# Performance work log

Measured on AMD Instinct MI355X. Metric: run time of the kernel, lower is better.

The kernel has to match this reference:

```python
import jax, jax.numpy as jnp
import numpy as np

N, T, H, W, C = 8, 128, 32, 32, 3
HID = 128
CONV_F = 32
FLAT = H * W * CONV_F  # 32768


def setup_inputs() -> dict:
    key = jax.random.key(0)
    ks = jax.random.split(key, 8)
    def w(k, shape, fan_in):
        return jax.random.normal(k, shape, jnp.float32) / np.sqrt(fan_in)
    x = jax.random.normal(ks[0], (N, T, H, W, C), jnp.float32)
    done = jax.random.randint(ks[1], (N, T), 0, 2, jnp.int32)
    return {
        "x": x,
        "done": done,
        "conv_w": w(ks[2], (3, 3, C, CONV_F), 3 * 3 * C),
        "conv_b": jnp.zeros((CONV_F,), jnp.float32),
        "early_w": w(ks[3], (FLAT, HID), FLAT),
        "early_b": jnp.zeros((HID,), jnp.float32),
        "lstm_wx": w(ks[4], (HID, 4 * HID), HID),
        "lstm_wh": w(ks[5], (HID, 4 * HID), HID),
        "lstm_b": jnp.zeros((4 * HID,), jnp.float32),
        "out_w": w(ks[6], (HID, HID), HID),
        "out_b": jnp.zeros((HID,), jnp.float32),
    }


def _forward(x, done, conv_w, conv_b, early_w, early_b,
             lstm_wx, lstm_wh, lstm_b, out_w, out_b):
    n, t = x.shape[0], x.shape[1]
    # conv encoder over flattened (N*T) frames, SAME padding (flax nn.Conv default)
    xf = x.reshape(n * t, H, W, C)
    xf = jax.lax.conv_general_dilated(
        xf, conv_w, window_strides=(1, 1), padding="SAME",
        dimension_numbers=("NHWC", "HWIO", "NHWC")) + conv_b
    feat = xf.reshape(n, t, -1)  # [N, T, FLAT]
    # early MLP
    feat = jax.nn.relu(feat @ early_w + early_b)  # [N, T, HID]
    # reset-masked LSTM scan over time
    # pre-compute input gate projections for all steps (batched matmul)
    zx = feat @ lstm_wx + lstm_b  # [N, T, 4H]
    zx_t = jnp.swapaxes(zx, 0, 1)       # [T, N, 4H]
    done_t = jnp.swapaxes(done, 0, 1)   # [T, N]

    def step(carry, inp):
        c, h = carry
        zxt, dt = inp
        mask = (dt != 0)[:, None]
        c = jnp.where(mask, 0.0, c)
        h = jnp.where(mask, 0.0, h)
        z = zxt + h @ lstm_wh  # [N, 4H]
        i, f, g, o = jnp.split(z, 4, axis=-1)
        i = jax.nn.sigmoid(i)
        f = jax.nn.sigmoid(f)
        g = jnp.tanh(g)
        o = jax.nn.sigmoid(o)
        c = f * c + i * g
        h = o * jnp.tanh(c)
        return (c, h), h

    init = (jnp.zeros((n, HID), jnp.float32), jnp.zeros((n, HID), jnp.float32))
    (c_fin, h_fin), hs = jax.lax.scan(step, init, (zx_t, done_t))
    hs = jnp.swapaxes(hs, 0, 1)  # [N, T, HID]
    # output MLP
    y = jax.nn.relu(hs @ out_w + out_b)
    return c_fin, h_fin, y


def reference(x, done, conv_w, conv_b, early_w, early_b,
              lstm_wx, lstm_wh, lstm_b, out_w, out_b):
    return _forward(x, done, conv_w, conv_b, early_w, early_b,
                    lstm_wx, lstm_wh, lstm_b, out_w, out_b)
```

## Files before the change

kernel.cpp:

```cpp
#include <hip/hip_runtime.h>


typedef unsigned short ushort_t;
typedef short bf16x8 __attribute__((ext_vector_type(8)));
typedef float f32x4 __attribute__((ext_vector_type(4)));
typedef _Float16 h2 __attribute__((ext_vector_type(2)));

__device__ __forceinline__ ushort_t f2b(float f) {
  unsigned u = __float_as_uint(f);
  return (ushort_t)((u + 0x7fffu + ((u >> 16) & 1u)) >> 16);
}
__device__ __forceinline__ unsigned pack_h2(float a, float b) {
  union { _Float16 h[2]; unsigned u; } v;
  v.h[0] = (_Float16)a; v.h[1] = (_Float16)b; return v.u;
}
__device__ __forceinline__ float fsig(float x) {
  return 1.f / (1.f + exp2f(-1.44269504f * x));
}
__device__ __forceinline__ float ftanh(float x) {
  float e = exp2f(2.885390082f * x);
  return 1.f - 2.f / (e + 1.f);
}
__device__ __forceinline__ int nth_bit(unsigned long long m0, unsigned long long m1, int i) {
  int c0 = __popcll(m0);
  if (i < c0) {
    unsigned long long m = m0;
    for (int k = 0; k < i; k++) m &= m - 1;
    return __ffsll((long long)m) - 1;
  }
  i -= c0;
  unsigned long long m = m1;
  for (int k = 0; k < i; k++) m &= m - 1;
  return 64 + __ffsll((long long)m) - 1;
}

__global__ __launch_bounds__(128) void prep_build(
    const float* __restrict__ conv_w, const float* __restrict__ conv_b,
    const float* __restrict__ early_w, const float* __restrict__ eb,
    const float* __restrict__ wx, const float* __restrict__ wh,
    const float* __restrict__ ow,
    ushort_t* __restrict__ UT, ushort_t* __restrict__ wxT,
    unsigned* __restrict__ whT16, unsigned* __restrict__ owT16,
    float* __restrict__ bias2)
{
  const int tid = threadIdx.x;
  const int b = blockIdx.x;

  if (b >= 1024) {
    for (int i = (b - 1024) * 128 + tid; i < 131200; i += 128 * 128) {
      int j = i;
      if (j < 65536) { int n = j >> 7, k = j & 127; wxT[j] = f2b(wx[k * 512 + n]); continue; }
      j -= 65536;
      if (j < 32768) { int col = j >> 6, k2 = j & 63;
        whT16[j] = pack_h2(wh[(2 * k2) * 512 + col], wh[(2 * k2 + 1) * 512 + col]); continue; }
      j -= 32768;
      if (j < 32768) { int col = j >> 6, k2 = j & 63;
        owT16[j] = pack_h2(ow[(2 * k2) * 128 + col], ow[(2 * k2 + 1) * 128 + col]); continue; }
      j -= 32768;
      bias2[j] = eb[j];
    }
    return;
  }

  __shared__ float cw[864];
  const int p = b;
  for (int i = tid; i < 864; i += 128) cw[i] = conv_w[i];
  __syncthreads();
  const int hp = p >> 5, wp = p & 31;
  float a0 = 0.f, a1 = 0.f, a2 = 0.f;
  for (int kh = 0; kh < 3; kh++) {
    int h = hp - kh + 1; if ((unsigned)h >= 32u) continue;
    for (int kw = 0; kw < 3; kw++) {
      int w = wp - kw + 1; if ((unsigned)w >= 32u) continue;
      const float* wr = early_w + ((size_t)((h * 32 + w) * 32)) * 128 + tid;
      const float* cwp = cw + (kh * 3 + kw) * 96;
      #pragma unroll 8
      for (int f = 0; f < 32; f++) {
        float wv = wr[f * 128];
        a0 += cwp[f]      * wv;
        a1 += cwp[32 + f] * wv;
        a2 += cwp[64 + f] * wv;
      }
    }
  }
  size_t ub = (size_t)tid * 3072 + p * 3;
  UT[ub + 0] = f2b(a0); UT[ub + 1] = f2b(a1); UT[ub + 2] = f2b(a2);

  float cbs = 0.f;
  #pragma unroll 8
  for (int f = 0; f < 32; f++) cbs += __builtin_fabsf(conv_b[f]);
  if (cbs != 0.f && p < 32) {
    float part = 0.f;
    for (int pp = p * 32; pp < p * 32 + 32; pp++)
      for (int f = 0; f < 32; f++)
        part += conv_b[f] * early_w[(size_t)(pp * 32 + f) * 128 + tid];
    atomicAdd(&bias2[tid], part);
  }
}

__global__ __launch_bounds__(256) void feat_gemm(
    const float* __restrict__ x, const ushort_t* __restrict__ UT,
    float* __restrict__ partial)
{
  __shared__ short As[16 * 72];
  __shared__ short Bs[128 * 72];
  const int tid = threadIdx.x;
  const int m0 = blockIdx.x * 16;
  const int ks = blockIdx.y;
  const int wave = tid >> 6, lane = tid & 63;
  const int quad = lane >> 4, l15 = lane & 15;
  const int c0 = wave * 32;

  f32x4 acc0 = {0.f, 0.f, 0.f, 0.f};
  f32x4 acc1 = {0.f, 0.f, 0.f, 0.f};

  const int kend = ks * 384 + 384;
  for (int k0 = ks * 384; k0 < kend; k0 += 64) {
    __syncthreads();
    for (int s = tid; s < 1152; s += 256) {
      if (s < 128) {
        int row = s >> 3, t8 = s & 7;
        const float4* g = (const float4*)(x + (size_t)(m0 + row) * 3072 + k0 + t8 * 8);
        float4 f0 = g[0], f1 = g[1];
        ushort_t tmp[8] = {f2b(f0.x), f2b(f0.y), f2b(f0.z), f2b(f0.w),
                           f2b(f1.x), f2b(f1.y), f2b(f1.z), f2b(f1.w)};
        *(uint4*)&As[row * 72 + t8 * 8] = *(const uint4*)tmp;
      } else {
        int s2 = s - 128;
        int row = s2 >> 3, t8 = s2 & 7;
        const uint4* g = (const uint4*)(UT + (size_t)row * 3072 + k0 + t8 * 8);
        *(uint4*)&Bs[row * 72 + t8 * 8] = *g;
      }
    }
    __syncthreads();
    #pragma unroll
    for (int kk = 0; kk < 2; kk++) {
      int ko = kk * 32 + quad * 8;
      bf16x8 a  = *(const bf16x8*)&As[l15 * 72 + ko];
      bf16x8 b0 = *(const bf16x8*)&Bs[(c0 + l15) * 72 + ko];
      bf16x8 b1 = *(const bf16x8*)&Bs[(c0 + 16 + l15) * 72 + ko];
      acc0 = __builtin_amdgcn_mfma_f32_16x16x32_bf16(a, b0, acc0, 0, 0, 0);
      acc1 = __builtin_amdgcn_mfma_f32_16x16x32_bf16(a, b1, acc1, 0, 0, 0);
    }
  }
  #pragma unroll
  for (int r = 0; r < 4; r++) {
    int m = m0 + quad * 4 + r;
    size_t base = ((size_t)ks * 1024 + m) * 128;
    partial[base + c0 + l15]      = acc0[r];
    partial[base + c0 + 16 + l15] = acc1[r];
  }
}

__global__ __launch_bounds__(256) void zx_gemm(
    const float* __restrict__ partial, const float* __restrict__ bias2,
    const ushort_t* __restrict__ wxT, const float* __restrict__ lstm_b,
    float* __restrict__ zx)
{
  __shared__ short As[16 * 136];
  __shared__ short Bs[128 * 136];
  const int tid = threadIdx.x;
  const int m0 = blockIdx.x * 16;
  const int n0 = blockIdx.y * 128;
  const int wave = tid >> 6, lane = tid & 63;
  const int quad = lane >> 4, l15 = lane & 15;
  const int c0 = wave * 32;

  {
    int r = tid >> 4, gA = tid & 15, cb = gA * 8;
    float4 s0 = {0,0,0,0}, s1 = {0,0,0,0};
    #pragma unroll
    for (int ks = 0; ks < 8; ks++) {
      const float4* p = (const float4*)(partial + (size_t)ks * 131072 + (m0 + r) * 128 + cb);
      float4 u0 = p[0], u1 = p[1];
      s0.x += u0.x; s0.y += u0.y; s0.z += u0.z; s0.w += u0.w;
      s1.x += u1.x; s1.y += u1.y; s1.z += u1.z; s1.w += u1.w;
    }
    const float* bp = bias2 + cb;
    union { ushort_t us[8]; uint4 v; } t8;
    t8.us[0] = f2b(fmaxf(s0.x + bp[0], 0.f)); t8.us[1] = f2b(fmaxf(s0.y + bp[1], 0.f));
    t8.us[2] = f2b(fmaxf(s0.z + bp[2], 0.f)); t8.us[3] = f2b(fmaxf(s0.w + bp[3], 0.f));
    t8.us[4] = f2b(fmaxf(s1.x + bp[4], 0.f)); t8.us[5] = f2b(fmaxf(s1.y + bp[5], 0.f));
    t8.us[6] = f2b(fmaxf(s1.z + bp[6], 0.f)); t8.us[7] = f2b(fmaxf(s1.w + bp[7], 0.f));
    *(uint4*)&As[r * 136 + gA * 8] = t8.v;
  }
  #pragma unroll
  for (int j = 0; j < 8; j++) {
    int s = tid + 256 * j, row = s >> 4, g = s & 15;
    uint4 v = *(const uint4*)(wxT + (size_t)(n0 + row) * 128 + g * 8);
    *(uint4*)&Bs[row * 136 + g * 8] = v;
  }
  __syncthreads();

  f32x4 acc0 = {0,0,0,0}, acc1 = {0,0,0,0};
  #pragma unroll
  for (int kk = 0; kk < 4; kk++) {
    int ko = kk * 32 + quad * 8;
    bf16x8 a  = *(const bf16x8*)&As[l15 * 136 + ko];
    bf16x8 b0 = *(const bf16x8*)&Bs[(c0 + l15) * 136 + ko];
    bf16x8 b1 = *(const bf16x8*)&Bs[(c0 + 16 + l15) * 136 + ko];
    acc0 = __builtin_amdgcn_mfma_f32_16x16x32_bf16(a, b0, acc0, 0, 0, 0);
    acc1 = __builtin_amdgcn_mfma_f32_16x16x32_bf16(a, b1, acc1, 0, 0, 0);
  }
  #pragma unroll
  for (int r = 0; r < 4; r++) {
    int m = m0 + quad * 4 + r;
    int n1 = n0 + c0 + l15, n2 = n1 + 16;
    zx[(size_t)m * 512 + n1] = acc0[r] + lstm_b[n1];
    zx[(size_t)m * 512 + n2] = acc1[r] + lstm_b[n2];
  }
}

__global__ __launch_bounds__(512, 1) void lstm_scan(
    const int* __restrict__ done, const float* __restrict__ zx,
    const unsigned* __restrict__ whT16, const unsigned* __restrict__ owT16,
    const float* __restrict__ out_b, float* __restrict__ dout)
{
  __shared__ float z_s[512];
  __shared__ float c_s[128];
  __shared__ _Float16 h16_s[128];
  __shared__ unsigned long long masks[16];
  const int tid = threadIdx.x;

  uint4 w4[16];
  {
    const uint4* wp = (const uint4*)(whT16 + (size_t)tid * 64);
    #pragma unroll
    for (int i = 0; i < 16; i++) w4[i] = wp[i];
  }
  const h2* wv = (const h2*)w4;

  uint4 o4[16];
  if (tid < 128) {
    const uint4* op = (const uint4*)(owT16 + (size_t)tid * 64);
    #pragma unroll
    for (int i = 0; i < 16; i++) o4[i] = op[i];
  }
  const h2* ov = (const h2*)o4;
  const float ob = (tid < 128) ? out_b[tid] : 0.f;

  for (int n = 0; n < 8; n++) {
    bool flag = false;
    if (tid < 128) flag = (tid == 0) || (done[n * 128 + tid] != 0);
    unsigned long long m = __ballot(flag);
    if (tid == 0)  masks[2 * n]     = m;
    if (tid == 64) masks[2 * n + 1] = m;
  }
  __syncthreads();

  int total = 0;
  #pragma unroll
  for (int n = 0; n < 8; n++)
    total += __popcll(masks[2 * n]) + __popcll(masks[2 * n + 1]);

  for (int g = blockIdx.x; g < total; g += gridDim.x) {
    int i = g, n = 0, cn = 0;
    for (; n < 8; n++) {
      cn = __popcll(masks[2 * n]) + __popcll(masks[2 * n + 1]);
      if (i < cn) break;
      i -= cn;
    }
    int t0 = nth_bit(masks[2 * n], masks[2 * n + 1], i);
    int t1 = (i + 1 < cn) ? nth_bit(masks[2 * n], masks[2 * n + 1], i + 1) : 128;

    if (tid < 128) { ((ushort_t*)h16_s)[tid] = 0; c_s[tid] = 0.f; }
    __syncthreads();

    for (int t = t0; t < t1; t++) {
      float zval = zx[((size_t)n * 128 + t) * 512 + tid];
      float a0 = 0.f, a1 = 0.f, a2 = 0.f, a3 = 0.f;
      const float4* hp = (const float4*)h16_s;
      #pragma unroll
      for (int q = 0; q < 16; q++) {
        float4 hb = hp[q];
        const h2* hh = (const h2*)&hb;
        a0 = __builtin_amdgcn_fdot2(wv[4*q+0], hh[0], a0, false);
        a1 = __builtin_amdgcn_fdot2(wv[4*q+1], hh[1], a1, false);
        a2 = __builtin_amdgcn_fdot2(wv[4*q+2], hh[2], a2, false);
        a3 = __builtin_amdgcn_fdot2(wv[4*q+3], hh[3], a3, false);
      }
      z_s[tid] = zval + (a0 + a1) + (a2 + a3);
      __syncthreads();
      if (tid < 128) {
        float ig = fsig(z_s[tid]);
        float fg = fsig(z_s[tid + 128]);
        float gg = ftanh(z_s[tid + 256]);
        float og = fsig(z_s[tid + 384]);
        float c = fg * c_s[tid] + ig * gg;
        float hn = og * ftanh(c);
        c_s[tid] = c;
        h16_s[tid] = (_Float16)hn;
        if (t == 127) {
          dout[n * 128 + tid] = c;
          dout[1024 + n * 128 + tid] = hn;
        }
      }
      __syncthreads();
      if (tid < 128) {
        float y0 = 0.f, y1 = 0.f, y2 = 0.f, y3 = 0.f;
        const float4* hq = (const float4*)h16_s;
        #pragma unroll
        for (int q = 0; q < 16; q++) {
          float4 hb = hq[q];
          const h2* hh = (const h2*)&hb;
          y0 = __builtin_amdgcn_fdot2(ov[4*q+0], hh[0], y0, false);
          y1 = __builtin_amdgcn_fdot2(ov[4*q+1], hh[1], y1, false);
          y2 = __builtin_amdgcn_fdot2(ov[4*q+2], hh[2], y2, false);
          y3 = __builtin_amdgcn_fdot2(ov[4*q+3], hh[3], y3, false);
        }
        dout[2048 + ((size_t)n * 128 + t) * 128 + tid] =
            fmaxf((y0 + y1) + (y2 + y3) + ob, 0.f);
      }
    }
  }
}

extern "C" void kernel_launch(void* const* d_in, const int* in_sizes, int n_in,
                              void* d_out, int out_size, void* d_ws, size_t ws_size,
                              hipStream_t stream) {
  const float* x       = (const float*)d_in[0];
  const int*   done    = (const int*)  d_in[1];
  const float* conv_w  = (const float*)d_in[2];
  const float* conv_b  = (const float*)d_in[3];
  const float* early_w = (const float*)d_in[4];
  const float* early_b = (const float*)d_in[5];
  const float* lstm_wx = (const float*)d_in[6];
  const float* lstm_wh = (const float*)d_in[7];
  const float* lstm_b  = (const float*)d_in[8];
  const float* out_w   = (const float*)d_in[9];
  const float* out_b   = (const float*)d_in[10];
  float* dout = (float*)d_out;

  char* ws = (char*)d_ws;
  float*    partial = (float*)   (ws + 0);
  ushort_t* UT      = (ushort_t*)(ws + 4194304);
  float*    zx      = (float*)   (ws + 4980736);
  ushort_t* wxT     = (ushort_t*)(ws + 7077888);
  unsigned* whT16   = (unsigned*)(ws + 7208960);
  unsigned* owT16   = (unsigned*)(ws + 7340032);
  float*    bias2   = (float*)   (ws + 7471104);

  prep_build<<<1152, 128, 0, stream>>>(conv_w, conv_b, early_w, early_b,
                                       lstm_wx, lstm_wh, out_w,
                                       UT, wxT, whT16, owT16, bias2);
  feat_gemm<<<dim3(64, 8), 256, 0, stream>>>(x, UT, partial);
  zx_gemm<<<dim3(64, 4), 256, 0, stream>>>(partial, bias2, wxT, lstm_b, zx);
  lstm_scan<<<512, 512, 0, stream>>>(done, zx, whT16, owT16, out_b, dout);
}
```

Before: 153.7 us.

## Restructure conv-folded weight build as scatter with atomics; double feat_gemm K-splits

The fused conv+early_w weight build moves from a gather form, where each output pixel re-reads nine neighbouring early_w slices from global memory, to a scatter form. Each block now loads its early_w slice into shared memory once and atomically adds contributions into an fp32 buffer, which a separate kernel then casts and transposes to bf16. The other weight transposes and the bias fold move into that cast kernel. Separately, the feat_gemm split-K count goes from 8 to 16 to raise parallelism, so zx_gemm sums twice as many partial buffers. The cost is an extra memset, two extra launches, float atomic traffic and a larger partial buffer.

```diff
diff --git a/kernel.cpp b/kernel.cpp
--- a/kernel.cpp
+++ b/kernel.cpp
@@ -5,6 +5,8 @@
 typedef short bf16x8 __attribute__((ext_vector_type(8)));
 typedef float f32x4 __attribute__((ext_vector_type(4)));
 typedef _Float16 h2 __attribute__((ext_vector_type(2)));
+
+#define KS 16
 
 __device__ __forceinline__ ushort_t f2b(float f) {
   unsigned u = __float_as_uint(f);
@@ -34,9 +36,48 @@
   return 64 + __ffsll((long long)m) - 1;
 }
 
-__global__ __launch_bounds__(128) void prep_build(
-    const float* __restrict__ conv_w, const float* __restrict__ conv_b,
-    const float* __restrict__ early_w, const float* __restrict__ eb,
+__global__ __launch_bounds__(128) void scatter_u(
+    const float* __restrict__ early_w, const float* __restrict__ conv_w,
+    float* __restrict__ Uf)
+{
+  __shared__ float ew_s[32 * 128];
+  __shared__ float cw[864];
+  const int tid = threadIdx.x;
+  const int q = blockIdx.x;
+
+  for (int i = tid; i < 864; i += 128) cw[i] = conv_w[i];
+  #pragma unroll 8
+  for (int f = 0; f < 32; f++)
+    ew_s[f * 128 + tid] = early_w[((size_t)(q * 32 + f)) * 128 + tid];
+  __syncthreads();
+
+  const int qh = q >> 5, qw = q & 31;
+  #pragma unroll
+  for (int kh = 0; kh < 3; kh++) {
+    int ph = qh + kh - 1; if ((unsigned)ph >= 32u) continue;
+    #pragma unroll
+    for (int kw = 0; kw < 3; kw++) {
+      int pw = qw + kw - 1; if ((unsigned)pw >= 32u) continue;
+      const float* c0p = &cw[(kh * 3 + kw) * 96];
+      float a0 = 0.f, a1 = 0.f, a2 = 0.f;
+      #pragma unroll 8
+      for (int f = 0; f < 32; f++) {
+        float e = ew_s[f * 128 + tid];
+        a0 += c0p[f]      * e;
+        a1 += c0p[32 + f] * e;
+        a2 += c0p[64 + f] * e;
+      }
+      int p = ph * 32 + pw;
+      atomicAdd(&Uf[(size_t)(p * 3 + 0) * 128 + tid], a0);
+      atomicAdd(&Uf[(size_t)(p * 3 + 1) * 128 + tid], a1);
+      atomicAdd(&Uf[(size_t)(p * 3 + 2) * 128 + tid], a2);
+    }
+  }
+}
+
+__global__ __launch_bounds__(256) void cast_prep(
+    const float* __restrict__ Uf, const float* __restrict__ eb,
+    const float* __restrict__ conv_b, const float* __restrict__ early_w,
     const float* __restrict__ wx, const float* __restrict__ wh,
     const float* __restrict__ ow,
     ushort_t* __restrict__ UT, ushort_t* __restrict__ wxT,
@@ -46,55 +87,35 @@
   const int tid = threadIdx.x;
   const int b = blockIdx.x;
 
-  if (b >= 1024) {
-    for (int i = (b - 1024) * 128 + tid; i < 131200; i += 128 * 128) {
-      int j = i;
-      if (j < 65536) { int n = j >> 7, k = j & 127; wxT[j] = f2b(wx[k * 512 + n]); continue; }
-      j -= 65536;
-      if (j < 32768) { int col = j >> 6, k2 = j & 63;
-        whT16[j] = pack_h2(wh[(2 * k2) * 512 + col], wh[(2 * k2 + 1) * 512 + col]); continue; }
-      j -= 32768;
-      if (j < 32768) { int col = j >> 6, k2 = j & 63;
-        owT16[j] = pack_h2(ow[(2 * k2) * 128 + col], ow[(2 * k2 + 1) * 128 + col]); continue; }
-      j -= 32768;
-      bias2[j] = eb[j];
-    }
+  if (b < 128) {
+    const int o = b;
+    const int k0 = tid * 12;
+    #pragma unroll
+    for (int k = k0; k < k0 + 12; k++)
+      UT[(size_t)o * 3072 + k] = f2b(Uf[(size_t)k * 128 + o]);
     return;
   }
-
-  __shared__ float cw[864];
-  const int p = b;
-  for (int i = tid; i < 864; i += 128) cw[i] = conv_w[i];
-  __syncthreads();
-  const int hp = p >> 5, wp = p & 31;
-  float a0 = 0.f, a1 = 0.f, a2 = 0.f;
-  for (int kh = 0; kh < 3; kh++) {
-    int h = hp - kh + 1; if ((unsigned)h >= 32u) continue;
-    for (int kw = 0; kw < 3; kw++) {
-      int w = wp - kw + 1; if ((unsigned)w >= 32u) continue;
-      const float* wr = early_w + ((size_t)((h * 32 + w) * 32)) * 128 + tid;
-      const float* cwp = cw + (kh * 3 + kw) * 96;
-      #pragma unroll 8
-      for (int f = 0; f < 32; f++) {
-        float wv = wr[f * 128];
-        a0 += cwp[f]      * wv;
-        a1 += cwp[32 + f] * wv;
-        a2 += cwp[64 + f] * wv;
-      }
-    }
-  }
-  size_t ub = (size_t)tid * 3072 + p * 3;
-  UT[ub + 0] = f2b(a0); UT[ub + 1] = f2b(a1); UT[ub + 2] = f2b(a2);
-
-  float cbs = 0.f;
-  #pragma unroll 8
-  for (int f = 0; f < 32; f++) cbs += __builtin_fabsf(conv_b[f]);
-  if (cbs != 0.f && p < 32) {
-    float part = 0.f;
-    for (int pp = p * 32; pp < p * 32 + 32; pp++)
-      for (int f = 0; f < 32; f++)
-        part += conv_b[f] * early_w[(size_t)(pp * 32 + f) * 128 + tid];
-    atomicAdd(&bias2[tid], part);
+  if (b < 640) {
+    int i = (b - 128) * 256 + tid;
+    if (i < 65536) { int n = i >> 7, k = i & 127; wxT[i] = f2b(wx[k * 512 + n]); return; }
+    i -= 65536;
+    if (i < 32768) { int col = i >> 6, k2 = i & 63;
+      whT16[i] = pack_h2(wh[(2 * k2) * 512 + col], wh[(2 * k2 + 1) * 512 + col]); return; }
+    i -= 32768;
+    { int col = i >> 6, k2 = i & 63;
+      owT16[i] = pack_h2(ow[(2 * k2) * 128 + col], ow[(2 * k2 + 1) * 128 + col]); }
+    return;
+  }
+  if (tid < 128) {
+    float s = eb[tid];
+    float cbs = 0.f;
+    for (int f = 0; f < 32; f++) cbs += __builtin_fabsf(conv_b[f]);
+    if (cbs != 0.f) {
+      for (int pp = 0; pp < 1024; pp++)
+        for (int f = 0; f < 32; f++)
+          s += conv_b[f] * early_w[(size_t)(pp * 32 + f) * 128 + tid];
+    }
+    bias2[tid] = s;
   }
 }
 
@@ -114,8 +135,8 @@
   f32x4 acc0 = {0.f, 0.f, 0.f, 0.f};
   f32x4 acc1 = {0.f, 0.f, 0.f, 0.f};
 
-  const int kend = ks * 384 + 384;
-  for (int k0 = ks * 384; k0 < kend; k0 += 64) {
+  const int kend = ks * 192 + 192;
+  for (int k0 = ks * 192; k0 < kend; k0 += 64) {
     __syncthreads();
     for (int s = tid; s < 1152; s += 256) {
       if (s < 128) {
@@ -170,7 +191,7 @@
     int r = tid >> 4, gA = tid & 15, cb = gA * 8;
     float4 s0 = {0,0,0,0}, s1 = {0,0,0,0};
     #pragma unroll
-    for (int ks = 0; ks < 8; ks++) {
+    for (int ks = 0; ks < KS; ks++) {
       const float4* p = (const float4*)(partial + (size_t)ks * 131072 + (m0 + r) * 128 + cb);
       float4 u0 = p[0], u1 = p[1];
       s0.x += u0.x; s0.y += u0.y; s0.z += u0.z; s0.w += u0.w;
@@ -333,17 +354,20 @@
 
   char* ws = (char*)d_ws;
   float*    partial = (float*)   (ws + 0);
-  ushort_t* UT      = (ushort_t*)(ws + 4194304);
-  float*    zx      = (float*)   (ws + 4980736);
-  ushort_t* wxT     = (ushort_t*)(ws + 7077888);
-  unsigned* whT16   = (unsigned*)(ws + 7208960);
-  unsigned* owT16   = (unsigned*)(ws + 7340032);
-  float*    bias2   = (float*)   (ws + 7471104);
-
-  prep_build<<<1152, 128, 0, stream>>>(conv_w, conv_b, early_w, early_b,
-                                       lstm_wx, lstm_wh, out_w,
-                                       UT, wxT, whT16, owT16, bias2);
-  feat_gemm<<<dim3(64, 8), 256, 0, stream>>>(x, UT, partial);
+  ushort_t* UT      = (ushort_t*)(ws + 8388608);
+  float*    Uf      = (float*)   (ws + 9175040);
+  float*    zx      = (float*)   (ws + 10747904);
+  ushort_t* wxT     = (ushort_t*)(ws + 12845056);
+  unsigned* whT16   = (unsigned*)(ws + 12976128);
+  unsigned* owT16   = (unsigned*)(ws + 13107200);
+  float*    bias2   = (float*)   (ws + 13139968);
+
+  hipMemsetAsync(Uf, 0, 3072 * 128 * 4, stream);
+  scatter_u<<<1024, 128, 0, stream>>>(early_w, conv_w, Uf);
+  cast_prep<<<641, 256, 0, stream>>>(Uf, early_b, conv_b, early_w,
+                                     lstm_wx, lstm_wh, out_w,
+                                     UT, wxT, whT16, owT16, bias2);
+  feat_gemm<<<dim3(64, KS), 256, 0, stream>>>(x, UT, partial);
   zx_gemm<<<dim3(64, 4), 256, 0, stream>>>(partial, bias2, wxT, lstm_b, zx);
   lstm_scan<<<512, 512, 0, stream>>>(done, zx, whT16, owT16, out_b, dout);
 }
```

New measurement: 148.3 us. 1.04x faster.
